# Kernel tuning notes

Hardware: AMD Instinct MI355X
Metric: run time of the kernel (lower is better)

## Reference

```python
import jax, jax.numpy as jnp
import numpy as np

D = 512
H = 8
G = 4          # GroupNorm groups
EPS = 1e-3     # GroupNorm eps


def group_norm(x):
    # x: (b, n, t, d); torch code normalizes per (batch, group) over (n*t, d/G)
    b, n, t, d = x.shape
    xr = x.reshape(b, n * t, G, d // G)
    mu = xr.mean(axis=(1, 3), keepdims=True)
    var = ((xr - mu) ** 2).mean(axis=(1, 3), keepdims=True)
    return ((xr - mu) * jax.lax.rsqrt(var + EPS)).reshape(b, n, t, d)


def setup_inputs() -> dict:
    key = jax.random.key(0)
    ks = jax.random.split(key, 9)
    s = 1.0 / np.sqrt(D)
    inp = {
        "ind": 0,
        "in_f": jax.random.normal(ks[0], (4, 8, 512, D), dtype=jnp.float32),
        "in_f_kv": jax.random.normal(ks[1], (4, 8, 512, D), dtype=jnp.float32),
        "Wq": jax.random.normal(ks[2], (D, D), dtype=jnp.float32) * s,
        "Wk": jax.random.normal(ks[3], (D, D), dtype=jnp.float32) * s,
        "Wv": jax.random.normal(ks[4], (D, D), dtype=jnp.float32) * s,
        "Wz": jax.random.normal(ks[5], (D, D), dtype=jnp.float32) * s,
        "bz": jnp.zeros((D,), dtype=jnp.float32),
        "W1": jax.random.normal(ks[6], (D, D), dtype=jnp.float32) * s,
        "b1": jnp.full((D,), 0.1, dtype=jnp.float32),
        "W2": jax.random.normal(ks[7], (D, D), dtype=jnp.float32) * s,
        "b2": jnp.full((D,), 0.1, dtype=jnp.float32),
    }
    return inp


def reference(ind, in_f, in_f_kv, Wq, Wk, Wv, Wz, bz, W1, b1, W2, b2):
    b, n, t, d = in_f.shape
    hd = d // H
    scale = 1.0 / np.sqrt(hd)

    _in_f = group_norm(in_f)          # LN_1
    _in_f_kv = group_norm(in_f_kv)    # LN_2

    # torch Linear: y = x @ W.T
    q = group_norm(_in_f @ Wq.T)      # LN_3
    k = group_norm(_in_f_kv @ Wk.T)   # LN_4
    v = _in_f_kv @ Wv.T

    q = q.reshape(b, n, t, H, hd)
    k = k.reshape(b, n, -1, H, hd)
    v = v.reshape(b, n, -1, H, hd)

    logits = jnp.einsum('bnqhd,bnkhd->bnhqk', q, k) * scale
    attn_weights = jax.nn.softmax(logits, axis=-1)
    attn_out = jnp.einsum('bnhqk,bnkhd->bnqhd', attn_weights, v).reshape(b, n, t, d)

    in_f_u1 = attn_out @ Wz.T + bz
    in_f_u2 = jax.nn.leaky_relu(_in_f @ W1.T + b1, negative_slope=0.01) @ W2.T + b2

    out_f = in_f + in_f_u1 + in_f_u2
    return (out_f, attn_weights)
```

## Files before the change

kernel.cpp:

```cpp
#include <hip/hip_runtime.h>
#include <math.h>

#define TDIM 512
#define DDIM 512
#define NTROWS 4096
#define MROWS 16384
#define EPSGN 1e-3f

typedef __attribute__((ext_vector_type(8))) short bf16x8;
typedef __attribute__((ext_vector_type(4))) float f32x4;
typedef __attribute__((ext_vector_type(8))) unsigned short us8;
typedef __attribute__((ext_vector_type(4))) unsigned short us4;

__device__ __forceinline__ unsigned short f2b(float f) {
  unsigned int u = __float_as_uint(f);
  return (unsigned short)((u + 0x7fffu + ((u >> 16) & 1u)) >> 16);
}
__device__ __forceinline__ float b2f(unsigned short h) {
  return __uint_as_float(((unsigned int)h) << 16);
}

#define GLOAD16(g, l)                                                                   \
  __builtin_amdgcn_global_load_lds((const __attribute__((address_space(1))) void*)(g),  \
                                   (__attribute__((address_space(3))) void*)(l), 16, 0, 0)

__global__ __launch_bounds__(256) void stats_cvt(const float* __restrict__ x0,
                                                 const float* __restrict__ x1,
                                                 unsigned short* __restrict__ o0,
                                                 unsigned short* __restrict__ o1,
                                                 float* __restrict__ p0,
                                                 float* __restrict__ p1) {
  const float* x = blockIdx.y ? x1 : x0;
  unsigned short* o = blockIdx.y ? o1 : o0;
  float* part = blockIdx.y ? p1 : p0;
  const int blk = blockIdx.x;
  const int batch = blk >> 6;
  const int chunk = blk & 63;
  const size_t base = (size_t)blk * 64 * 512;
  const int tid = threadIdx.x;
  float s = 0.f, sq = 0.f;
#pragma unroll 4
  for (int it = 0; it < 16; ++it) {
    const size_t e = base + (size_t)it * 2048 + (size_t)tid * 8;
    const float4 f0 = *(const float4*)(x + e);
    const float4 f1 = *(const float4*)(x + e + 4);
    us8 v;
    v[0] = f2b(f0.x); v[1] = f2b(f0.y); v[2] = f2b(f0.z); v[3] = f2b(f0.w);
    v[4] = f2b(f1.x); v[5] = f2b(f1.y); v[6] = f2b(f1.z); v[7] = f2b(f1.w);
    *(us8*)(o + e) = v;
    s += f0.x + f0.y + f0.z + f0.w + f1.x + f1.y + f1.z + f1.w;
    sq += f0.x * f0.x + f0.y * f0.y + f0.z * f0.z + f0.w * f0.w +
          f1.x * f1.x + f1.y * f1.y + f1.z * f1.z + f1.w * f1.w;
  }
  const int wave = tid >> 6, lane = tid & 63;
#pragma unroll
  for (int of = 1; of < 16; of <<= 1) { s += __shfl_xor(s, of); sq += __shfl_xor(sq, of); }
  __shared__ float red[4][4][2];
  if ((lane & 15) == 0) { red[wave][lane >> 4][0] = s; red[wave][lane >> 4][1] = sq; }
  __syncthreads();
  if (tid < 4) {
    float S = 0.f, SQ = 0.f;
#pragma unroll
    for (int w = 0; w < 4; ++w) { S += red[w][tid][0]; SQ += red[w][tid][1]; }
    const int idx = (((batch << 2) | tid) << 6) | chunk;
    part[idx * 2] = S;
    part[idx * 2 + 1] = SQ;
  }
}

__global__ __launch_bounds__(256) void wprep(const float* __restrict__ Wq,
                                             const float* __restrict__ Wk,
                                             const float* __restrict__ Wv,
                                             const float* __restrict__ W1,
                                             const float* __restrict__ Wz,
                                             const float* __restrict__ W2,
                                             const float* __restrict__ p0,
                                             const float* __restrict__ p1,
                                             unsigned short* __restrict__ w16s,
                                             float* __restrict__ corr) {
  const int y = blockIdx.y;
  if (y >= 16) {
    const float* s = (y == 16) ? Wz : W2;
    unsigned short* d = w16s + (size_t)y * 262144;
    const int c = blockIdx.x * 256 + threadIdx.x;
    const float4 f0 = *(const float4*)(s + (size_t)c * 8);
    const float4 f1 = *(const float4*)(s + (size_t)c * 8 + 4);
    us8 v;
    v[0] = f2b(f0.x); v[1] = f2b(f0.y); v[2] = f2b(f0.z); v[3] = f2b(f0.w);
    v[4] = f2b(f1.x); v[5] = f2b(f1.y); v[6] = f2b(f1.z); v[7] = f2b(f1.w);
    *(us8*)(d + (size_t)c * 8) = v;
    return;
  }
  const int w = y >> 2, b = y & 3;
  const float* W = (w == 0) ? Wq : (w == 1) ? Wk : (w == 2) ? Wv : W1;
  const float* part = (w == 0 || w == 3) ? p0 : p1;
  __shared__ float mrs[4][2];
  if (threadIdx.x < 4) {
    const float* p = part + (((b << 2) | threadIdx.x) << 6) * 2;
    float S = 0.f, SQ = 0.f;
    for (int c = 0; c < 64; ++c) { S += p[c * 2]; SQ += p[c * 2 + 1]; }
    const float inv = 1.f / (float)(NTROWS * 128);
    const float mu = S * inv;
    const float var = SQ * inv - mu * mu;
    const float rs = rsqrtf(var + EPSGN);
    mrs[threadIdx.x][0] = rs;
    mrs[threadIdx.x][1] = mu * rs;
  }
  __syncthreads();
  const int wave = threadIdx.x >> 6, lane = threadIdx.x & 63;
  const int n = blockIdx.x * 4 + wave;
  const int k = lane * 8;
  const int g = lane >> 4;
  const float rs = mrs[g][0], murs = mrs[g][1];
  const float4 f0 = *(const float4*)(W + (size_t)n * 512 + k);
  const float4 f1 = *(const float4*)(W + (size_t)n * 512 + k + 4);
  us8 v;
  v[0] = f2b(f0.x * rs); v[1] = f2b(f0.y * rs); v[2] = f2b(f0.z * rs); v[3] = f2b(f0.w * rs);
  v[4] = f2b(f1.x * rs); v[5] = f2b(f1.y * rs); v[6] = f2b(f1.z * rs); v[7] = f2b(f1.w * rs);
  *(us8*)(w16s + (size_t)((w << 2) | b) * 262144 + (size_t)n * 512 + k) = v;
  float t = (f0.x + f0.y + f0.z + f0.w + f1.x + f1.y + f1.z + f1.w) * murs;
#pragma unroll
  for (int of = 1; of < 64; of <<= 1) t += __shfl_xor(t, of);
  if (lane == 0) corr[(((w << 2) | b) << 9) | n] = t;
}

__global__ __launch_bounds__(256) void gemm_all(const unsigned short* __restrict__ a16,
                                                const unsigned short* __restrict__ akv16,
                                                const unsigned short* __restrict__ w16s,
                                                const float* __restrict__ corr,
                                                unsigned short* __restrict__ q16,
                                                unsigned short* __restrict__ h16,
                                                unsigned short* __restrict__ k16,
                                                unsigned short* __restrict__ vTb,
                                                const float* __restrict__ b1,
                                                float* __restrict__ part_q,
                                                float* __restrict__ part_k,
                                                float* __restrict__ sk) {
  __shared__ __align__(16) unsigned short As[128 * 64];
  __shared__ __align__(16) unsigned short Bs[128 * 64];
  __shared__ float red[8];
  const int tid = threadIdx.x;
  const int wave = tid >> 6, lane = tid & 63;
  const int bm = blockIdx.x << 7;
  const int batch = blockIdx.x >> 5;
  const int z = blockIdx.z;
  const bool first = blockIdx.y < 4;
  const int widx = z ? (first ? 1 : 2) : (first ? 0 : 3);
  const unsigned short* A = z ? akv16 : a16;
  const unsigned short* B = w16s + (size_t)262144 * ((widx << 2) | batch);
  const int bnl = (blockIdx.y & 3) << 7;
  const int wr = (wave >> 1) << 6;
  const int wc = (wave & 1) << 6;
  const int lr = lane & 15, lg = lane >> 4;

  f32x4 acc[4][4] = {};
  const int srow = lane >> 3;
  const int sslot = (lane & 7) ^ srow;

  for (int k0 = 0; k0 < 512; k0 += 64) {
    __syncthreads();
#pragma unroll
    for (int i = 0; i < 4; ++i) {
      const int ci = wave * 4 + i;
      const int row = ci * 8 + srow;
      GLOAD16(A + (size_t)(bm + row) * 512 + k0 + sslot * 8, (char*)As + ci * 1024);
      GLOAD16(B + (size_t)(bnl + row) * 512 + k0 + sslot * 8, (char*)Bs + ci * 1024);
    }
    __syncthreads();
#pragma unroll
    for (int kk = 0; kk < 64; kk += 32) {
      bf16x8 af[4], bfr[4];
#pragma unroll
      for (int i = 0; i < 4; ++i) {
        const int row = wr + i * 16 + lr;
        af[i] = *(const bf16x8*)&As[row * 64 + ((((kk >> 3) + lg) ^ (row & 7)) << 3)];
      }
#pragma unroll
      for (int j = 0; j < 4; ++j) {
        const int row = wc + j * 16 + lr;
        bfr[j] = *(const bf16x8*)&Bs[row * 64 + ((((kk >> 3) + lg) ^ (row & 7)) << 3)];
      }
#pragma unroll
      for (int i = 0; i < 4; ++i)
#pragma unroll
        for (int j = 0; j < 4; ++j)
          acc[i][j] = __builtin_amdgcn_mfma_f32_16x16x32_bf16(af[i], bfr[j], acc[i][j], 0, 0, 0);
    }
  }

  {
    const float* cb = corr + (((widx << 2) | batch) << 9);
    float cj[4];
#pragma unroll
    for (int j = 0; j < 4; ++j) cj[j] = cb[bnl + wc + j * 16 + lr];
#pragma unroll
    for (int i = 0; i < 4; ++i)
#pragma unroll
      for (int j = 0; j < 4; ++j)
#pragma unroll
        for (int r = 0; r < 4; ++r) acc[i][j][r] -= cj[j];
  }

  if (first) {
    unsigned short* C0 = z ? k16 : q16;
#pragma unroll
    for (int i = 0; i < 4; ++i) {
      const int row0 = bm + wr + i * 16 + lg * 4;
#pragma unroll
      for (int j = 0; j < 4; ++j) {
        const int col = bnl + wc + j * 16 + lr;
#pragma unroll
        for (int r = 0; r < 4; ++r)
          C0[(size_t)(row0 + r) * 512 + col] = f2b(acc[i][j][r]);
      }
    }
    float s = 0.f, sq = 0.f;
#pragma unroll
    for (int i = 0; i < 4; ++i)
#pragma unroll
      for (int j = 0; j < 4; ++j)
#pragma unroll
        for (int r = 0; r < 4; ++r) { const float v = acc[i][j][r]; s += v; sq += v * v; }
#pragma unroll
    for (int o = 32; o > 0; o >>= 1) { s += __shfl_xor(s, o); sq += __shfl_xor(sq, o); }
    if (lane == 0) { red[wave * 2] = s; red[wave * 2 + 1] = sq; }
    __syncthreads();
    if (tid == 0) {
      float* part = z ? part_k : part_q;
      const float S = red[0] + red[2] + red[4] + red[6];
      const float SQ = red[1] + red[3] + red[5] + red[7];
      const int slot = blockIdx.x & 31, g = blockIdx.y;
      const int idx = ((((batch << 2) | g) << 5) | slot) << 1;
      part[idx] = S;
      part[idx + 1] = SQ;
    }
    if (z) {
      const int head = (bnl >> 6) + (wave & 1);
#pragma unroll
      for (int i = 0; i < 4; ++i) {
#pragma unroll
        for (int r = 0; r < 4; ++r) {
          float t = acc[i][0][r] + acc[i][1][r] + acc[i][2][r] + acc[i][3][r];
#pragma unroll
          for (int o = 1; o < 16; o <<= 1) t += __shfl_xor(t, o);
          if (lr == 0)
            sk[(size_t)(bm + wr + i * 16 + lg * 4 + r) * 8 + head] = t;
        }
      }
    }
  } else if (z == 0) {
#pragma unroll
    for (int i = 0; i < 4; ++i) {
      const int row0 = bm + wr + i * 16 + lg * 4;
#pragma unroll
      for (int j = 0; j < 4; ++j) {
        const int col = bnl + wc + j * 16 + lr;
        const float bb = b1[col];
#pragma unroll
        for (int r = 0; r < 4; ++r) {
          float v = acc[i][j][r] + bb;
          v = v > 0.f ? v : 0.01f * v;
          h16[(size_t)(row0 + r) * 512 + col] = f2b(v);
        }
      }
    }
  } else {
#pragma unroll
    for (int i = 0; i < 4; ++i) {
      const int row0 = bm + wr + i * 16 + lg * 4;
#pragma unroll
      for (int j = 0; j < 4; ++j) {
        const int col = bnl + wc + j * 16 + lr;
        us4 pk;
#pragma unroll
        for (int r = 0; r < 4; ++r) pk[r] = f2b(acc[i][j][r]);
        *(us4*)&vTb[((size_t)(row0 >> 9) * 512 + col) * 512 + (row0 & 511)] = pk;
      }
    }
  }
}

__global__ __launch_bounds__(256) void gemm_final(const unsigned short* __restrict__ A0,
                                                  const unsigned short* __restrict__ A1,
                                                  const unsigned short* __restrict__ B0,
                                                  const unsigned short* __restrict__ B1,
                                                  float* __restrict__ Cf,
                                                  const float* __restrict__ bias0,
                                                  const float* __restrict__ bias1,
                                                  const unsigned short* __restrict__ init16) {
  __shared__ __align__(16) unsigned short As[128 * 64];
  __shared__ __align__(16) unsigned short Bs[128 * 64];
  const int tid = threadIdx.x;
  const int wave = tid >> 6, lane = tid & 63;
  const int bm = blockIdx.x << 7, bn = blockIdx.y << 7;
  const int wr = (wave >> 1) << 6;
  const int wc = (wave & 1) << 6;
  const int lr = lane & 15, lg = lane >> 4;

  f32x4 acc[4][4] = {};
  const int srow = lane >> 3;
  const int sslot = (lane & 7) ^ srow;

  for (int k0 = 0; k0 < 1024; k0 += 64) {
    const unsigned short* Ab = (k0 < 512) ? A0 : A1;
    const unsigned short* Bb = (k0 < 512) ? B0 : B1;
    const int kl = k0 & 511;
    __syncthreads();
#pragma unroll
    for (int i = 0; i < 4; ++i) {
      const int ci = wave * 4 + i;
      const int row = ci * 8 + srow;
      GLOAD16(Ab + (size_t)(bm + row) * 512 + kl + sslot * 8, (char*)As + ci * 1024);
      GLOAD16(Bb + (size_t)(bn + row) * 512 + kl + sslot * 8, (char*)Bs + ci * 1024);
    }
    __syncthreads();
#pragma unroll
    for (int kk = 0; kk < 64; kk += 32) {
      bf16x8 af[4], bfr[4];
#pragma unroll
      for (int i = 0; i < 4; ++i) {
        const int row = wr + i * 16 + lr;
        af[i] = *(const bf16x8*)&As[row * 64 + ((((kk >> 3) + lg) ^ (row & 7)) << 3)];
      }
#pragma unroll
      for (int j = 0; j < 4; ++j) {
        const int row = wc + j * 16 + lr;
        bfr[j] = *(const bf16x8*)&Bs[row * 64 + ((((kk >> 3) + lg) ^ (row & 7)) << 3)];
      }
#pragma unroll
      for (int i = 0; i < 4; ++i)
#pragma unroll
        for (int j = 0; j < 4; ++j)
          acc[i][j] = __builtin_amdgcn_mfma_f32_16x16x32_bf16(af[i], bfr[j], acc[i][j], 0, 0, 0);
    }
  }

#pragma unroll
  for (int i = 0; i < 4; ++i) {
    const int row0 = bm + wr + i * 16 + lg * 4;
#pragma unroll
    for (int j = 0; j < 4; ++j) {
      const int col = bn + wc + j * 16 + lr;
      const float bb = bias0[col] + bias1[col];
#pragma unroll
      for (int r = 0; r < 4; ++r) {
        const size_t o = (size_t)(row0 + r) * 512 + col;
        Cf[o] = acc[i][j][r] + bb + b2f(init16[o]);
      }
    }
  }
}

__global__ __launch_bounds__(256) void attn_fused(const unsigned short* __restrict__ q16,
                                                  const unsigned short* __restrict__ k16,
                                                  const unsigned short* __restrict__ vT,
                                                  const float* __restrict__ part_q,
                                                  const float* __restrict__ part_k,
                                                  const float* __restrict__ sk,
                                                  float* __restrict__ aw,
                                                  unsigned short* __restrict__ ao16) {
  __shared__ __align__(16) unsigned short Qs[64 * 64];
  __shared__ __align__(16) unsigned short Ks[256 * 64];
  __shared__ __align__(16) unsigned short Ps[64 * 256];
  __shared__ float WM[4][64];
  __shared__ float WS[4][64];
  __shared__ float sk_lds[512];
  __shared__ float cst[2];

  const int bid = blockIdx.x;
  const int q0 = blockIdx.y << 6;
  const int h = bid & 7;
  const int b = bid >> 6;
  const int tid = threadIdx.x;
  const int w = tid >> 6, lane = tid & 63;
  const int lr = lane & 15, lg = lane >> 4;
  const int srow = lane >> 3;
  const int sslot = (lane & 7) ^ srow;

  const size_t hb = (size_t)(bid >> 3) * (512 * 512);
  const unsigned short* Qg = q16 + hb + h * 64;
  const unsigned short* Kg = k16 + hb + h * 64;
  const unsigned short* Vg = vT + hb + (size_t)h * 64 * 512;

  if (tid == 0) {
    const int pbase = (((b << 2) | (h >> 1)) << 6);
    const float* pq = part_q + pbase;
    const float* pk = part_k + pbase;
    float Sq = 0.f, SQq = 0.f, Sk = 0.f, SQk = 0.f;
    for (int c = 0; c < 32; ++c) {
      Sq += pq[c * 2]; SQq += pq[c * 2 + 1];
      Sk += pk[c * 2]; SQk += pk[c * 2 + 1];
    }
    const float inv = 1.f / (float)(NTROWS * 128);
    const float muq = Sq * inv, vq = SQq * inv - muq * muq;
    const float muk = Sk * inv, vk = SQk * inv - muk * muk;
    const float a = rsqrtf(vq + EPSGN) * rsqrtf(vk + EPSGN) * 0.125f;
    cst[0] = a;
    cst[1] = a * muq;
  }
  {
    const float* skg = sk + (size_t)(bid >> 3) * 512 * 8 + h;
    for (int j = tid; j < 512; j += 256) sk_lds[j] = skg[(size_t)j * 8];
  }

#pragma unroll
  for (int it = 0; it < 2; ++it) {
    const int ci = w * 2 + it;
    const int row = ci * 8 + srow;
    GLOAD16(Qg + (size_t)(q0 + row) * 512 + sslot * 8, (char*)Qs + ci * 1024);
  }

  f32x4 sc[4][8] = {};

#pragma unroll
  for (int half = 0; half < 2; ++half) {
    __syncthreads();
#pragma unroll
    for (int it = 0; it < 8; ++it) {
      const int ci = w * 8 + it;
      const int row = ci * 8 + srow;
      GLOAD16(Kg + (size_t)(half * 256 + row) * 512 + sslot * 8, (char*)Ks + ci * 1024);
    }
    __syncthreads();
#pragma unroll
    for (int kk = 0; kk < 64; kk += 32) {
      bf16x8 aq[4];
#pragma unroll
      for (int qf = 0; qf < 4; ++qf) {
        const int row = qf * 16 + lr;
        aq[qf] = *(const bf16x8*)&Qs[row * 64 + ((((kk >> 3) + lg) ^ (row & 7)) << 3)];
      }
#pragma unroll
      for (int kf = 0; kf < 4; ++kf) {
        const int row = w * 64 + kf * 16 + lr;
        const bf16x8 bk = *(const bf16x8*)&Ks[row * 64 + ((((kk >> 3) + lg) ^ (row & 7)) << 3)];
#pragma unroll
        for (int qf = 0; qf < 4; ++qf)
          sc[qf][half * 4 + kf] =
              __builtin_amdgcn_mfma_f32_16x16x32_bf16(aq[qf], bk, sc[qf][half * 4 + kf], 0, 0, 0);
      }
    }
  }

  const float aSc = cst[0], cmu = cst[1];
#pragma unroll
  for (int qf = 0; qf < 4; ++qf)
#pragma unroll
    for (int kfi = 0; kfi < 8; ++kfi) {
      const int k = ((kfi >> 2) << 8) + w * 64 + ((kfi & 3) << 4) + lr;
      const float corr = cmu * sk_lds[k];
#pragma unroll
      for (int r = 0; r < 4; ++r) sc[qf][kfi][r] = aSc * sc[qf][kfi][r] - corr;
    }

  float Mv[4][4];
#pragma unroll
  for (int qf = 0; qf < 4; ++qf)
#pragma unroll
    for (int r = 0; r < 4; ++r) {
      float m = sc[qf][0][r];
#pragma unroll
      for (int kf = 1; kf < 8; ++kf) m = fmaxf(m, sc[qf][kf][r]);
#pragma unroll
      for (int o = 1; o < 16; o <<= 1) m = fmaxf(m, __shfl_xor(m, o));
      Mv[qf][r] = m;
    }
  if (lr == 0) {
#pragma unroll
    for (int qf = 0; qf < 4; ++qf)
#pragma unroll
      for (int r = 0; r < 4; ++r) WM[w][qf * 16 + lg * 4 + r] = Mv[qf][r];
  }
  __syncthreads();
#pragma unroll
  for (int qf = 0; qf < 4; ++qf)
#pragma unroll
    for (int r = 0; r < 4; ++r) {
      const int q = qf * 16 + lg * 4 + r;
      Mv[qf][r] = fmaxf(fmaxf(WM[0][q], WM[1][q]), fmaxf(WM[2][q], WM[3][q]));
    }
  float sl[4][4] = {};
#pragma unroll
  for (int qf = 0; qf < 4; ++qf)
#pragma unroll
    for (int kf = 0; kf < 8; ++kf) {
      f32x4 v = sc[qf][kf];
#pragma unroll
      for (int r = 0; r < 4; ++r) {
        const float e = __expf(v[r] - Mv[qf][r]);
        v[r] = e;
        sl[qf][r] += e;
      }
      sc[qf][kf] = v;
    }
#pragma unroll
  for (int qf = 0; qf < 4; ++qf)
#pragma unroll
    for (int r = 0; r < 4; ++r) {
      float s = sl[qf][r];
#pragma unroll
      for (int o = 1; o < 16; o <<= 1) s += __shfl_xor(s, o);
      sl[qf][r] = s;
    }
  if (lr == 0) {
#pragma unroll
    for (int qf = 0; qf < 4; ++qf)
#pragma unroll
      for (int r = 0; r < 4; ++r) WS[w][qf * 16 + lg * 4 + r] = sl[qf][r];
  }
  __syncthreads();
#pragma unroll
  for (int qf = 0; qf < 4; ++qf)
#pragma unroll
    for (int r = 0; r < 4; ++r) {
      const int q = qf * 16 + lg * 4 + r;
      const float inv = 1.f / (WS[0][q] + WS[1][q] + WS[2][q] + WS[3][q]);
#pragma unroll
      for (int kf = 0; kf < 8; ++kf) sc[qf][kf][r] *= inv;
    }

  float* AWp = aw + ((size_t)bid * 512 + q0) * 512;
#pragma unroll
  for (int qf = 0; qf < 4; ++qf)
#pragma unroll
    for (int kfi = 0; kfi < 8; ++kfi) {
      const int k = ((kfi >> 2) << 8) + w * 64 + ((kfi & 3) << 4) + lr;
#pragma unroll
      for (int r = 0; r < 4; ++r)
        __builtin_nontemporal_store(sc[qf][kfi][r],
                                    &AWp[(size_t)(qf * 16 + lg * 4 + r) * 512 + k]);
    }

  f32x4 accO[4] = {};
#pragma unroll
  for (int half = 0; half < 2; ++half) {
    __syncthreads();
#pragma unroll
    for (int it = 0; it < 8; ++it) {
      const int ci = w * 8 + it;
      const int row = ci * 2 + (lane >> 5);
      const int s = lane & 31;
      GLOAD16(Vg + (size_t)row * 512 + half * 256 + ((s ^ (row & 7)) << 3),
              (char*)Ks + ci * 1024);
    }
#pragma unroll
    for (int qf = 0; qf < 4; ++qf)
#pragma unroll
      for (int r = 0; r < 4; ++r) {
        const int q = qf * 16 + lg * 4 + r;
#pragma unroll
        for (int kf = 0; kf < 4; ++kf) {
          const int k = w * 64 + (kf << 4) + lr;
          Ps[q * 256 + (((k >> 3) ^ (q & 7)) << 3) + (k & 7)] = f2b(sc[qf][half * 4 + kf][r]);
        }
      }
    __syncthreads();
#pragma unroll
    for (int ks = 0; ks < 256; ks += 32) {
      const int sl0 = ks >> 3;
      const int q = w * 16 + lr;
      const bf16x8 af = *(const bf16x8*)&Ps[q * 256 + (((sl0 + lg) ^ (q & 7)) << 3)];
#pragma unroll
      for (int df = 0; df < 4; ++df) {
        const int row = df * 16 + lr;
        const bf16x8 vb = *(const bf16x8*)&Ks[row * 256 + (((sl0 + lg) ^ (row & 7)) << 3)];
        accO[df] = __builtin_amdgcn_mfma_f32_16x16x32_bf16(af, vb, accO[df], 0, 0, 0);
      }
    }
  }

  const int growb = (bid >> 3) * 512 + q0 + w * 16 + lg * 4;
#pragma unroll
  for (int df = 0; df < 4; ++df)
#pragma unroll
    for (int r = 0; r < 4; ++r)
      ao16[(size_t)(growb + r) * 512 + h * 64 + df * 16 + lr] = f2b(accO[df][r]);
}

extern "C" void kernel_launch(void* const* d_in, const int* in_sizes, int n_in,
                              void* d_out, int out_size, void* d_ws, size_t ws_size,
                              hipStream_t stream) {
  const float* in_f = (const float*)d_in[1];
  const float* in_fkv = (const float*)d_in[2];
  const float* Wq = (const float*)d_in[3];
  const float* Wk = (const float*)d_in[4];
  const float* Wv = (const float*)d_in[5];
  const float* Wz = (const float*)d_in[6];
  const float* bz = (const float*)d_in[7];
  const float* W1 = (const float*)d_in[8];
  const float* b1 = (const float*)d_in[9];
  const float* W2 = (const float*)d_in[10];
  const float* b2 = (const float*)d_in[11];

  float* out_f = (float*)d_out;
  float* attw = out_f + (size_t)MROWS * DDIM;

  const size_t TSB = (size_t)MROWS * DDIM;
  unsigned short* us = (unsigned short*)d_ws;
  unsigned short* a16 = us;
  unsigned short* akv16 = us + TSB;
  unsigned short* q16 = us + 2 * TSB;
  unsigned short* k16 = us + 3 * TSB;
  unsigned short* h16 = us + 4 * TSB;
  unsigned short* ao16 = us + 5 * TSB;
  unsigned short* vT = us + 6 * TSB;
  unsigned short* w16s = us + 7 * TSB;
  float* fbase = (float*)(us + 7 * TSB + 18 * 262144);
  float* p0 = fbase;
  float* p1 = fbase + 2048;
  float* part_q = fbase + 4096;
  float* part_k = fbase + 5120;
  float* corr = fbase + 6144;
  float* sk = fbase + 14336;

  stats_cvt<<<dim3(256, 2), 256, 0, stream>>>(in_f, in_fkv, a16, akv16, p0, p1);
  wprep<<<dim3(128, 18), 256, 0, stream>>>(Wq, Wk, Wv, W1, Wz, W2, p0, p1, w16s, corr);
  gemm_all<<<dim3(128, 8, 2), 256, 0, stream>>>(a16, akv16, w16s, corr, q16, h16, k16, vT, b1,
                                                part_q, part_k, sk);
  attn_fused<<<dim3(256, 8), 256, 0, stream>>>(q16, k16, vT, part_q, part_k, sk, attw, ao16);
  gemm_final<<<dim3(128, 4), 256, 0, stream>>>(ao16, h16, w16s + 16 * 262144,
                                               w16s + 17 * 262144, out_f, bz, b2, a16);
}
```

Before: 241.1 us.

## Prefetch V early in attention, split stats into more blocks, move weight casts

The attention kernel now issues the first half of the V tile load into LDS before the softmax work, so the global-to-LDS copy runs underneath the softmax arithmetic and the attention-weight stores. The PV loop is unrolled into two explicit halves. The stats/convert kernel uses twice as many blocks with half the rows each, doubling the partial-sum count that wprep reduces. The Wz/W2 bf16 conversion moves from wprep into a third y-slice of the stats kernel. Together these aim to hide V load latency and improve occupancy in the first pass, at the cost of a longer serial reduction in wprep and a reshuffled workspace layout.

```diff
diff --git a/kernel.cpp b/kernel.cpp
--- a/kernel.cpp
+++ b/kernel.cpp
@@ -29,18 +29,37 @@
                                                  unsigned short* __restrict__ o0,
                                                  unsigned short* __restrict__ o1,
                                                  float* __restrict__ p0,
-                                                 float* __restrict__ p1) {
+                                                 float* __restrict__ p1,
+                                                 const float* __restrict__ Wz,
+                                                 const float* __restrict__ W2,
+                                                 unsigned short* __restrict__ w16s) {
+  if (blockIdx.y == 2) {
+    const int bid = blockIdx.x;
+    if (bid >= 256) return;
+    const int c = bid * 256 + threadIdx.x;
+    const int t = c >> 15;
+    const int off = c & 32767;
+    const float* s = t ? W2 : Wz;
+    unsigned short* d = w16s + (size_t)(16 + t) * 262144;
+    const float4 f0 = *(const float4*)(s + (size_t)off * 8);
+    const float4 f1 = *(const float4*)(s + (size_t)off * 8 + 4);
+    us8 v;
+    v[0] = f2b(f0.x); v[1] = f2b(f0.y); v[2] = f2b(f0.z); v[3] = f2b(f0.w);
+    v[4] = f2b(f1.x); v[5] = f2b(f1.y); v[6] = f2b(f1.z); v[7] = f2b(f1.w);
+    *(us8*)(d + (size_t)off * 8) = v;
+    return;
+  }
   const float* x = blockIdx.y ? x1 : x0;
   unsigned short* o = blockIdx.y ? o1 : o0;
   float* part = blockIdx.y ? p1 : p0;
   const int blk = blockIdx.x;
-  const int batch = blk >> 6;
-  const int chunk = blk & 63;
-  const size_t base = (size_t)blk * 64 * 512;
+  const int batch = blk >> 7;
+  const int chunk = blk & 127;
+  const size_t base = (size_t)blk * 32 * 512;
   const int tid = threadIdx.x;
   float s = 0.f, sq = 0.f;
 #pragma unroll 4
-  for (int it = 0; it < 16; ++it) {
+  for (int it = 0; it < 8; ++it) {
     const size_t e = base + (size_t)it * 2048 + (size_t)tid * 8;
     const float4 f0 = *(const float4*)(x + e);
     const float4 f1 = *(const float4*)(x + e + 4);
@@ -62,7 +81,7 @@
     float S = 0.f, SQ = 0.f;
 #pragma unroll
     for (int w = 0; w < 4; ++w) { S += red[w][tid][0]; SQ += red[w][tid][1]; }
-    const int idx = (((batch << 2) | tid) << 6) | chunk;
+    const int idx = (((batch << 2) | tid) << 7) | chunk;
     part[idx * 2] = S;
     part[idx * 2 + 1] = SQ;
   }
@@ -72,33 +91,19 @@
                                              const float* __restrict__ Wk,
                                              const float* __restrict__ Wv,
                                              const float* __restrict__ W1,
-                                             const float* __restrict__ Wz,
-                                             const float* __restrict__ W2,
                                              const float* __restrict__ p0,
                                              const float* __restrict__ p1,
                                              unsigned short* __restrict__ w16s,
                                              float* __restrict__ corr) {
   const int y = blockIdx.y;
-  if (y >= 16) {
-    const float* s = (y == 16) ? Wz : W2;
-    unsigned short* d = w16s + (size_t)y * 262144;
-    const int c = blockIdx.x * 256 + threadIdx.x;
-    const float4 f0 = *(const float4*)(s + (size_t)c * 8);
-    const float4 f1 = *(const float4*)(s + (size_t)c * 8 + 4);
-    us8 v;
-    v[0] = f2b(f0.x); v[1] = f2b(f0.y); v[2] = f2b(f0.z); v[3] = f2b(f0.w);
-    v[4] = f2b(f1.x); v[5] = f2b(f1.y); v[6] = f2b(f1.z); v[7] = f2b(f1.w);
-    *(us8*)(d + (size_t)c * 8) = v;
-    return;
-  }
   const int w = y >> 2, b = y & 3;
   const float* W = (w == 0) ? Wq : (w == 1) ? Wk : (w == 2) ? Wv : W1;
   const float* part = (w == 0 || w == 3) ? p0 : p1;
   __shared__ float mrs[4][2];
   if (threadIdx.x < 4) {
-    const float* p = part + (((b << 2) | threadIdx.x) << 6) * 2;
+    const float* p = part + (((b << 2) | threadIdx.x) << 7) * 2;
     float S = 0.f, SQ = 0.f;
-    for (int c = 0; c < 64; ++c) { S += p[c * 2]; SQ += p[c * 2 + 1]; }
+    for (int c = 0; c < 128; ++c) { S += p[c * 2]; SQ += p[c * 2 + 1]; }
     const float inv = 1.f / (float)(NTROWS * 128);
     const float mu = S * inv;
     const float var = SQ * inv - mu * mu;
@@ -442,6 +447,14 @@
     }
   }
 
+#pragma unroll
+  for (int it = 0; it < 8; ++it) {
+    const int ci = w * 8 + it;
+    const int row = ci * 2 + (lane >> 5);
+    const int s = lane & 31;
+    GLOAD16(Vg + (size_t)row * 512 + ((s ^ (row & 7)) << 3), (char*)Ks + ci * 1024);
+  }
+
   const float aSc = cst[0], cmu = cst[1];
 #pragma unroll
   for (int qf = 0; qf < 4; ++qf)
@@ -531,41 +544,64 @@
                                     &AWp[(size_t)(qf * 16 + lg * 4 + r) * 512 + k]);
     }
 
+#pragma unroll
+  for (int qf = 0; qf < 4; ++qf)
+#pragma unroll
+    for (int r = 0; r < 4; ++r) {
+      const int q = qf * 16 + lg * 4 + r;
+#pragma unroll
+      for (int kf = 0; kf < 4; ++kf) {
+        const int k = w * 64 + (kf << 4) + lr;
+        Ps[q * 256 + (((k >> 3) ^ (q & 7)) << 3) + (k & 7)] = f2b(sc[qf][kf][r]);
+      }
+    }
+  __syncthreads();
+
   f32x4 accO[4] = {};
 #pragma unroll
-  for (int half = 0; half < 2; ++half) {
-    __syncthreads();
-#pragma unroll
-    for (int it = 0; it < 8; ++it) {
-      const int ci = w * 8 + it;
-      const int row = ci * 2 + (lane >> 5);
-      const int s = lane & 31;
-      GLOAD16(Vg + (size_t)row * 512 + half * 256 + ((s ^ (row & 7)) << 3),
-              (char*)Ks + ci * 1024);
-    }
-#pragma unroll
-    for (int qf = 0; qf < 4; ++qf)
-#pragma unroll
-      for (int r = 0; r < 4; ++r) {
-        const int q = qf * 16 + lg * 4 + r;
-#pragma unroll
-        for (int kf = 0; kf < 4; ++kf) {
-          const int k = w * 64 + (kf << 4) + lr;
-          Ps[q * 256 + (((k >> 3) ^ (q & 7)) << 3) + (k & 7)] = f2b(sc[qf][half * 4 + kf][r]);
-        }
-      }
-    __syncthreads();
-#pragma unroll
-    for (int ks = 0; ks < 256; ks += 32) {
-      const int sl0 = ks >> 3;
-      const int q = w * 16 + lr;
-      const bf16x8 af = *(const bf16x8*)&Ps[q * 256 + (((sl0 + lg) ^ (q & 7)) << 3)];
-#pragma unroll
-      for (int df = 0; df < 4; ++df) {
-        const int row = df * 16 + lr;
-        const bf16x8 vb = *(const bf16x8*)&Ks[row * 256 + (((sl0 + lg) ^ (row & 7)) << 3)];
-        accO[df] = __builtin_amdgcn_mfma_f32_16x16x32_bf16(af, vb, accO[df], 0, 0, 0);
-      }
+  for (int ks = 0; ks < 256; ks += 32) {
+    const int sl0 = ks >> 3;
+    const int q = w * 16 + lr;
+    const bf16x8 af = *(const bf16x8*)&Ps[q * 256 + (((sl0 + lg) ^ (q & 7)) << 3)];
+#pragma unroll
+    for (int df = 0; df < 4; ++df) {
+      const int row = df * 16 + lr;
+      const bf16x8 vb = *(const bf16x8*)&Ks[row * 256 + (((sl0 + lg) ^ (row & 7)) << 3)];
+      accO[df] = __builtin_amdgcn_mfma_f32_16x16x32_bf16(af, vb, accO[df], 0, 0, 0);
+    }
+  }
+  __syncthreads();
+
+#pragma unroll
+  for (int it = 0; it < 8; ++it) {
+    const int ci = w * 8 + it;
+    const int row = ci * 2 + (lane >> 5);
+    const int s = lane & 31;
+    GLOAD16(Vg + (size_t)row * 512 + 256 + ((s ^ (row & 7)) << 3), (char*)Ks + ci * 1024);
+  }
+#pragma unroll
+  for (int qf = 0; qf < 4; ++qf)
+#pragma unroll
+    for (int r = 0; r < 4; ++r) {
+      const int q = qf * 16 + lg * 4 + r;
+#pragma unroll
+      for (int kf = 0; kf < 4; ++kf) {
+        const int k = w * 64 + (kf << 4) + lr;
+        Ps[q * 256 + (((k >> 3) ^ (q & 7)) << 3) + (k & 7)] = f2b(sc[qf][4 + kf][r]);
+      }
+    }
+  __syncthreads();
+
+#pragma unroll
+  for (int ks = 0; ks < 256; ks += 32) {
+    const int sl0 = ks >> 3;
+    const int q = w * 16 + lr;
+    const bf16x8 af = *(const bf16x8*)&Ps[q * 256 + (((sl0 + lg) ^ (q & 7)) << 3)];
+#pragma unroll
+    for (int df = 0; df < 4; ++df) {
+      const int row = df * 16 + lr;
+      const bf16x8 vb = *(const bf16x8*)&Ks[row * 256 + (((sl0 + lg) ^ (row & 7)) << 3)];
+      accO[df] = __builtin_amdgcn_mfma_f32_16x16x32_bf16(af, vb, accO[df], 0, 0, 0);
     }
   }
 
@@ -607,14 +643,14 @@
   unsigned short* w16s = us + 7 * TSB;
   float* fbase = (float*)(us + 7 * TSB + 18 * 262144);
   float* p0 = fbase;
-  float* p1 = fbase + 2048;
-  float* part_q = fbase + 4096;
-  float* part_k = fbase + 5120;
-  float* corr = fbase + 6144;
-  float* sk = fbase + 14336;
-
-  stats_cvt<<<dim3(256, 2), 256, 0, stream>>>(in_f, in_fkv, a16, akv16, p0, p1);
-  wprep<<<dim3(128, 18), 256, 0, stream>>>(Wq, Wk, Wv, W1, Wz, W2, p0, p1, w16s, corr);
+  float* p1 = fbase + 4096;
+  float* part_q = fbase + 8192;
+  float* part_k = fbase + 9216;
+  float* corr = fbase + 10240;
+  float* sk = fbase + 18432;
+
+  stats_cvt<<<dim3(512, 3), 256, 0, stream>>>(in_f, in_fkv, a16, akv16, p0, p1, Wz, W2, w16s);
+  wprep<<<dim3(128, 16), 256, 0, stream>>>(Wq, Wk, Wv, W1, p0, p1, w16s, corr);
   gemm_all<<<dim3(128, 8, 2), 256, 0, stream>>>(a16, akv16, w16s, corr, q16, h16, k16, vT, b1,
                                                 part_q, part_k, sk);
   attn_fused<<<dim3(256, 8), 256, 0, stream>>>(q16, k16, vT, part_q, part_k, sk, attw, ao16);
```

Measured after the change: 239.1 us. About the same (-0.9%).
